# Kernel optimization log

Hardware: AMD Instinct MI355X
Metric: run time of the kernel (lower is better)

Reference implementation:

```python
import jax, jax.numpy as jnp
import numpy as np

C = 64
CQ = C // 8


def setup_inputs() -> dict:
    key = jax.random.key(0)
    ks = jax.random.split(key, 8)
    scale = 0.05
    x = jax.random.normal(ks[0], (4, C, 64, 64), dtype=jnp.float32)
    Wq = jax.random.normal(ks[1], (CQ, C), dtype=jnp.float32) * scale
    bq = jax.random.normal(ks[2], (CQ,), dtype=jnp.float32) * scale
    Wk = jax.random.normal(ks[3], (CQ, C), dtype=jnp.float32) * scale
    bk = jax.random.normal(ks[4], (CQ,), dtype=jnp.float32) * scale
    Wv = jax.random.normal(ks[5], (C, C), dtype=jnp.float32) * scale
    bv = jax.random.normal(ks[6], (C,), dtype=jnp.float32) * scale
    gamma = jnp.zeros((1,), dtype=jnp.float32) + 0.5  # nonzero so output depends on attention
    return {"x": x, "Wq": Wq, "bq": bq, "Wk": Wk, "bk": bk, "Wv": Wv, "bv": bv, "gamma": gamma}


def reference(x, Wq, bq, Wk, bk, Wv, bv, gamma):
    bs, c, h, w = x.shape
    hw = h * w
    xf = x.reshape(bs, c, hw)  # [b, c, hw]
    # 1x1 convs == per-pixel linear over channels
    Q = jnp.einsum('oc,bcn->bon', Wq, xf) + bq[None, :, None]  # [b, c/8, hw]
    K = jnp.einsum('oc,bcn->bon', Wk, xf) + bk[None, :, None]  # [b, c/8, hw]
    V = jnp.einsum('oc,bcn->bon', Wv, xf) + bv[None, :, None]  # [b, c, hw]
    # attention = softmax(Q^T K, axis=-1), NO scaling (matches source)
    scores = jnp.einsum('bqn,bqm->bnm', Q, K)  # [b, hw, hw]
    attn = jax.nn.softmax(scores, axis=-1)
    out = jnp.einsum('bcm,bmn->bcn', V, attn)  # torch.bmm(V_, attention)
    out = out.reshape(bs, c, h, w)
    return gamma[0] * out + x
```

## Files before the change

### kernel.cpp

```cpp
#include <hip/hip_runtime.h>


constexpr int Bn = 4, Cc = 64, Q8 = 8, Np = 4096;
constexpr int QK_STR = 32;
constexpr int PSTR = 40;
constexpr int NSL = 4;
constexpr int KSTR = 40;

typedef float f32x4 __attribute__((ext_vector_type(4)));
typedef short short8 __attribute__((ext_vector_type(8)));

__device__ inline unsigned int f2bf(float x) {
    unsigned int u = __float_as_uint(x);
    u += 0x7fff + ((u >> 16) & 1);
    return u >> 16;
}
__device__ inline float bf2f(unsigned int u) { return __uint_as_float(u << 16); }

__global__ __launch_bounds__(64) void qkv_v2(
    const float* __restrict__ x,
    const float* __restrict__ Wq, const float* __restrict__ bq,
    const float* __restrict__ Wk, const float* __restrict__ bk,
    const float* __restrict__ Wv, const float* __restrict__ bv,
    unsigned short* __restrict__ Qp, unsigned short* __restrict__ Kp,
    unsigned short* __restrict__ Vb)
{
    const int lane = threadIdx.x;
    const int gpos = blockIdx.x * 64;
    const int os = blockIdx.y;
    const int b = gpos >> 12, n = (gpos & (Np - 1)) + lane;

    float xv[Cc];
    const float* xp = x + (size_t)(b * Cc) * Np + n;
    #pragma unroll
    for (int c = 0; c < Cc; c++) xv[c] = xp[(size_t)c * Np];

    if (os == 0) {
        unsigned pk[4];
        float a0, a1;
        #pragma unroll
        for (int p = 0; p < 4; p++) {
            a0 = bq[2 * p]; a1 = bq[2 * p + 1];
            #pragma unroll
            for (int c = 0; c < Cc; c++) {
                a0 += Wq[(2 * p) * Cc + c] * xv[c];
                a1 += Wq[(2 * p + 1) * Cc + c] * xv[c];
            }
            pk[p] = f2bf(a0) | (f2bf(a1) << 16);
        }
        unsigned short* qrow = Qp + (size_t)(b * Np + n) * QK_STR;
        *(uint4*)qrow = make_uint4(pk[0], pk[1], pk[2], pk[3]);
        *(uint4*)(qrow + 8)  = make_uint4(0, 0, 0, 0);
        *(uint4*)(qrow + 16) = make_uint4(0, 0, 0, 0);
        *(uint4*)(qrow + 24) = make_uint4(0, 0, 0, 0);
        #pragma unroll
        for (int p = 0; p < 4; p++) {
            a0 = bk[2 * p]; a1 = bk[2 * p + 1];
            #pragma unroll
            for (int c = 0; c < Cc; c++) {
                a0 += Wk[(2 * p) * Cc + c] * xv[c];
                a1 += Wk[(2 * p + 1) * Cc + c] * xv[c];
            }
            pk[p] = f2bf(a0) | (f2bf(a1) << 16);
        }
        unsigned short* krow = Kp + (size_t)(b * Np + n) * QK_STR;
        *(uint4*)krow = make_uint4(pk[0], pk[1], pk[2], pk[3]);
        *(uint4*)(krow + 8)  = make_uint4(0, 0, 0, 0);
        *(uint4*)(krow + 16) = make_uint4(0, 0, 0, 0);
        *(uint4*)(krow + 24) = make_uint4(0, 0, 0, 0);
        #pragma unroll
        for (int o = 0; o < 4; o++) {
            float a = bv[o];
            #pragma unroll
            for (int c = 0; c < Cc; c++) a += Wv[o * Cc + c] * xv[c];
            Vb[(size_t)(b * Cc + o) * Np + n] = (unsigned short)f2bf(a);
        }
    } else {
        const int vbase = os * 20 - 16;
        #pragma unroll 4
        for (int o = 0; o < 20; o++) {
            const int vr = vbase + o;
            float a = bv[vr];
            #pragma unroll
            for (int c = 0; c < Cc; c++) a += Wv[vr * Cc + c] * xv[c];
            Vb[(size_t)(b * Cc + vr) * Np + n] = (unsigned short)f2bf(a);
        }
    }
}

__global__ __launch_bounds__(256) void zsum_v2(
    const unsigned short* __restrict__ Qp, const unsigned short* __restrict__ Kp,
    float* __restrict__ ZP)
{
    __shared__ unsigned short Klds[64 * KSTR];
    const int tid = threadIdx.x, w = tid >> 6, lane = tid & 63;
    const int quad = lane >> 4, l15 = lane & 15;
    const int bz = blockIdx.z, ns = blockIdx.y;
    const int m0 = blockIdx.x * 64 + w * 16;

    short8 qa = *(const short8*)&Qp[((size_t)(bz * Np + m0 + l15)) * QK_STR + quad * 8];

    const int rt = tid >> 2, ct = tid & 3;
    const int nbase = ns * (Np / NSL);
    const unsigned short* kbase = Kp + (size_t)bz * Np * QK_STR;

    uint4 pf = *(const uint4*)&kbase[(size_t)(nbase + rt) * QK_STR + ct * 8];
    float z0 = 0.f, z1 = 0.f, z2 = 0.f, z3 = 0.f;
    for (int nt = 0; nt < Np / NSL; nt += 64) {
        *(uint4*)&Klds[rt * KSTR + ct * 8] = pf;
        __syncthreads();
        if (nt + 64 < Np / NSL)
            pf = *(const uint4*)&kbase[(size_t)(nbase + nt + 64 + rt) * QK_STR + ct * 8];
        #pragma unroll
        for (int t16 = 0; t16 < 4; t16++) {
            short8 kb = *(const short8*)&Klds[(t16 * 16 + l15) * KSTR + quad * 8];
            f32x4 s = __builtin_amdgcn_mfma_f32_16x16x32_bf16(
                qa, kb, f32x4{0.f, 0.f, 0.f, 0.f}, 0, 0, 0);
            z0 += __expf(s[0]); z1 += __expf(s[1]);
            z2 += __expf(s[2]); z3 += __expf(s[3]);
        }
        __syncthreads();
    }
    #pragma unroll
    for (int mask = 1; mask < 16; mask <<= 1) {
        z0 += __shfl_xor(z0, mask); z1 += __shfl_xor(z1, mask);
        z2 += __shfl_xor(z2, mask); z3 += __shfl_xor(z3, mask);
    }
    if (l15 == 0) {
        float4 v = make_float4(z0, z1, z2, z3);
        *(float4*)&ZP[((size_t)(bz * NSL + ns)) * Np + m0 + quad * 4] = v;
    }
}

__global__ __launch_bounds__(256) void zred(
    const float* __restrict__ ZP, float* __restrict__ Zinv)
{
    int i = blockIdx.x * 256 + threadIdx.x;
    int b = i >> 12, m = i & (Np - 1);
    float z = 0.f;
    #pragma unroll
    for (int s = 0; s < NSL; s++) z += ZP[((size_t)(b * NSL + s)) * Np + m];
    Zinv[(size_t)b * Np + m] = 1.f / z;
}

__global__ __launch_bounds__(256) void attn_mfma(
    const unsigned short* __restrict__ Qp, const unsigned short* __restrict__ Kp,
    const unsigned short* __restrict__ Vb, const float* __restrict__ Zinv,
    unsigned short* __restrict__ PO, int Ms, int SL)
{
    __shared__ unsigned short Plds[128 * PSTR];
    const int tid = threadIdx.x, w = tid >> 6, lane = tid & 63;
    const int quad = lane >> 4, l15 = lane & 15;
    const int bz = blockIdx.z, by = blockIdx.y, nb = blockIdx.x * 128;

    short8 kf[2];
    #pragma unroll
    for (int t = 0; t < 2; t++) {
        int n = nb + (2 * w + t) * 16 + l15;
        kf[t] = *(const short8*)&Kp[((size_t)(bz * Np + n)) * QK_STR + quad * 8];
    }
    f32x4 acc[4][2];
    #pragma unroll
    for (int ct = 0; ct < 4; ct++)
        #pragma unroll
        for (int t = 0; t < 2; t++) acc[ct][t] = f32x4{0.f, 0.f, 0.f, 0.f};

    const int m_base = by * Ms;
    for (int mi = 0; mi < Ms; mi += 32) {
        const int m0 = m_base + mi;
        #pragma unroll
        for (int mt = 0; mt < 2; mt++) {
            short8 qa = *(const short8*)
                &Qp[((size_t)(bz * Np + m0 + mt * 16 + l15)) * QK_STR + quad * 8];
            float4 zi = *(const float4*)
                &Zinv[(size_t)bz * Np + m0 + mt * 16 + quad * 4];
            #pragma unroll
            for (int t = 0; t < 2; t++) {
                f32x4 s = __builtin_amdgcn_mfma_f32_16x16x32_bf16(
                    qa, kf[t], f32x4{0.f, 0.f, 0.f, 0.f}, 0, 0, 0);
                unsigned e0 = f2bf(__expf(s[0]) * zi.x), e1 = f2bf(__expf(s[1]) * zi.y);
                unsigned e2 = f2bf(__expf(s[2]) * zi.z), e3 = f2bf(__expf(s[3]) * zi.w);
                int nl = (2 * w + t) * 16 + l15;
                *(uint2*)&Plds[nl * PSTR + mt * 16 + quad * 4] =
                    make_uint2(e0 | (e1 << 16), e2 | (e3 << 16));
            }
        }
        short8 pb[2];
        #pragma unroll
        for (int t = 0; t < 2; t++)
            pb[t] = *(const short8*)&Plds[(w * 32 + t * 16 + l15) * PSTR + quad * 8];
        #pragma unroll
        for (int ct = 0; ct < 4; ct++) {
            short8 ua = *(const short8*)
                &Vb[((size_t)(bz * Cc + ct * 16 + l15)) * Np + m0 + quad * 8];
            #pragma unroll
            for (int t = 0; t < 2; t++)
                acc[ct][t] = __builtin_amdgcn_mfma_f32_16x16x32_bf16(
                    ua, pb[t], acc[ct][t], 0, 0, 0);
        }
    }
    unsigned short* po = PO + ((size_t)((bz * SL + by) * Cc)) * Np + nb;
    #pragma unroll
    for (int ct = 0; ct < 4; ct++)
        #pragma unroll
        for (int t = 0; t < 2; t++) {
            int c = ct * 16 + quad * 4, n = w * 32 + t * 16 + l15;
            #pragma unroll
            for (int r = 0; r < 4; r++)
                po[(size_t)(c + r) * Np + n] = (unsigned short)f2bf(acc[ct][t][r]);
        }
}

__global__ __launch_bounds__(256) void combine_kernel(
    const unsigned short* __restrict__ PO, const float* __restrict__ x,
    const float* __restrict__ gamma, float* __restrict__ out, int sl2)
{
    int idx8 = (blockIdx.x * 256 + threadIdx.x) * 8;
    int b = idx8 >> 18;
    int c = (idx8 >> 12) & 63;
    int n = idx8 & (Np - 1);
    float o[8];
    #pragma unroll
    for (int i = 0; i < 8; i++) o[i] = 0.f;
    for (int sl = 0; sl < sl2; ++sl) {
        uint4 u = *(const uint4*)&PO[(size_t)((b * sl2 + sl) * Cc + c) * Np + n];
        o[0] += bf2f(u.x & 0xffff); o[1] += bf2f(u.x >> 16);
        o[2] += bf2f(u.y & 0xffff); o[3] += bf2f(u.y >> 16);
        o[4] += bf2f(u.z & 0xffff); o[5] += bf2f(u.z >> 16);
        o[6] += bf2f(u.w & 0xffff); o[7] += bf2f(u.w >> 16);
    }
    float g = gamma[0];
    float4 x0 = *(const float4*)&x[idx8];
    float4 x1 = *(const float4*)&x[idx8 + 4];
    float4 r0 = make_float4(g * o[0] + x0.x, g * o[1] + x0.y,
                            g * o[2] + x0.z, g * o[3] + x0.w);
    float4 r1 = make_float4(g * o[4] + x1.x, g * o[5] + x1.y,
                            g * o[6] + x1.z, g * o[7] + x1.w);
    *(float4*)&out[idx8] = r0;
    *(float4*)&out[idx8 + 4] = r1;
}

extern "C" void kernel_launch(void* const* d_in, const int* in_sizes, int n_in,
                              void* d_out, int out_size, void* d_ws, size_t ws_size,
                              hipStream_t stream)
{
    const float* x     = (const float*)d_in[0];
    const float* Wq    = (const float*)d_in[1];
    const float* bq    = (const float*)d_in[2];
    const float* Wk    = (const float*)d_in[3];
    const float* bk    = (const float*)d_in[4];
    const float* Wv    = (const float*)d_in[5];
    const float* bv    = (const float*)d_in[6];
    const float* gamma = (const float*)d_in[7];
    float* out = (float*)d_out;

    unsigned short* Qp = (unsigned short*)d_ws;
    unsigned short* Kp = Qp + (size_t)Bn * Np * QK_STR;
    unsigned short* Vb = Kp + (size_t)Bn * Np * QK_STR;
    float* Zinv = (float*)(Vb + (size_t)Bn * Cc * Np);
    float* ZP   = Zinv + (size_t)Bn * Np;
    unsigned short* PO = (unsigned short*)(ZP + (size_t)Bn * NSL * Np);

    size_t baseB = (size_t)Bn * Np * QK_STR * 2 * 2 + (size_t)Bn * Cc * Np * 2
                 + (size_t)Bn * Np * 4 + (size_t)Bn * NSL * Np * 4;
    int SL = 4;
    while (SL > 1 && baseB + (size_t)Bn * SL * Cc * Np * 2 > ws_size) SL >>= 1;

    qkv_v2<<<dim3(Bn * Np / 64, 4), 64, 0, stream>>>(x, Wq, bq, Wk, bk, Wv, bv,
                                                     Qp, Kp, Vb);
    zsum_v2<<<dim3(Np / 64, NSL, Bn), 256, 0, stream>>>(Qp, Kp, ZP);
    zred<<<Bn * Np / 256, 256, 0, stream>>>(ZP, Zinv);
    attn_mfma<<<dim3(Np / 128, SL, Bn), 256, 0, stream>>>(Qp, Kp, Vb, Zinv,
                                                          PO, Np / SL, SL);
    combine_kernel<<<Bn * Cc * Np / (256 * 8), 256, 0, stream>>>(PO, x, gamma, out, SL);
}
```

Measured before the change: 149.4 us.

## Fold softmax normalizer into MFMA accumulator via log2 and halve attn tile

Q is prescaled by log2(e) so exponentials become native exp2, and the per-row normalizer is stored as -log2(Z) and fed as the MFMA accumulator init, which removes the separate multiply by 1/Z. Packing to bf16 now uses the hardware v_cvt_pk_bf16_f32 instruction instead of manual rounding. The attention block drops from 128 to 64 columns, so each wave handles a single 16-column tile, which doubles the block count but halves per-wave work and also doubles the reloads of Q and V across blocks.

```diff
diff --git a/kernel.cpp b/kernel.cpp
--- a/kernel.cpp
+++ b/kernel.cpp
@@ -16,6 +16,26 @@
     return u >> 16;
 }
 __device__ inline float bf2f(unsigned int u) { return __uint_as_float(u << 16); }
+
+__device__ inline unsigned cvt_pk_bf16(float a, float b) {
+    unsigned r;
+    asm("v_cvt_pk_bf16_f32 %0, %1, %2" : "=v"(r) : "v"(a), "v"(b));
+    return r;
+}
+__device__ inline float exp2g(float x) {
+#if __has_builtin(__builtin_amdgcn_exp2f)
+    return __builtin_amdgcn_exp2f(x);
+#else
+    return exp2f(x);
+#endif
+}
+__device__ inline float log2g(float x) {
+#if __has_builtin(__builtin_amdgcn_logf)
+    return __builtin_amdgcn_logf(x);
+#else
+    return log2f(x);
+#endif
+}
 
 __global__ __launch_bounds__(64) void qkv_v2(
     const float* __restrict__ x,
@@ -29,6 +49,7 @@
     const int gpos = blockIdx.x * 64;
     const int os = blockIdx.y;
     const int b = gpos >> 12, n = (gpos & (Np - 1)) + lane;
+    const float LOG2E = 1.4426950408889634f;
 
     float xv[Cc];
     const float* xp = x + (size_t)(b * Cc) * Np + n;
@@ -46,7 +67,7 @@
                 a0 += Wq[(2 * p) * Cc + c] * xv[c];
                 a1 += Wq[(2 * p + 1) * Cc + c] * xv[c];
             }
-            pk[p] = f2bf(a0) | (f2bf(a1) << 16);
+            pk[p] = f2bf(a0 * LOG2E) | (f2bf(a1 * LOG2E) << 16);
         }
         unsigned short* qrow = Qp + (size_t)(b * Np + n) * QK_STR;
         *(uint4*)qrow = make_uint4(pk[0], pk[1], pk[2], pk[3]);
@@ -116,8 +137,8 @@
             short8 kb = *(const short8*)&Klds[(t16 * 16 + l15) * KSTR + quad * 8];
             f32x4 s = __builtin_amdgcn_mfma_f32_16x16x32_bf16(
                 qa, kb, f32x4{0.f, 0.f, 0.f, 0.f}, 0, 0, 0);
-            z0 += __expf(s[0]); z1 += __expf(s[1]);
-            z2 += __expf(s[2]); z3 += __expf(s[3]);
+            z0 += exp2g(s[0]); z1 += exp2g(s[1]);
+            z2 += exp2g(s[2]); z3 += exp2g(s[3]);
         }
         __syncthreads();
     }
@@ -133,37 +154,32 @@
 }
 
 __global__ __launch_bounds__(256) void zred(
-    const float* __restrict__ ZP, float* __restrict__ Zinv)
+    const float* __restrict__ ZP, float* __restrict__ Lg)
 {
     int i = blockIdx.x * 256 + threadIdx.x;
     int b = i >> 12, m = i & (Np - 1);
     float z = 0.f;
     #pragma unroll
     for (int s = 0; s < NSL; s++) z += ZP[((size_t)(b * NSL + s)) * Np + m];
-    Zinv[(size_t)b * Np + m] = 1.f / z;
-}
-
-__global__ __launch_bounds__(256) void attn_mfma(
+    Lg[(size_t)b * Np + m] = -log2g(z);
+}
+
+__global__ __launch_bounds__(256) void attn_v2(
     const unsigned short* __restrict__ Qp, const unsigned short* __restrict__ Kp,
-    const unsigned short* __restrict__ Vb, const float* __restrict__ Zinv,
+    const unsigned short* __restrict__ Vb, const float* __restrict__ Lg,
     unsigned short* __restrict__ PO, int Ms, int SL)
 {
-    __shared__ unsigned short Plds[128 * PSTR];
+    __shared__ unsigned short Plds[64 * PSTR];
     const int tid = threadIdx.x, w = tid >> 6, lane = tid & 63;
     const int quad = lane >> 4, l15 = lane & 15;
-    const int bz = blockIdx.z, by = blockIdx.y, nb = blockIdx.x * 128;
-
-    short8 kf[2];
-    #pragma unroll
-    for (int t = 0; t < 2; t++) {
-        int n = nb + (2 * w + t) * 16 + l15;
-        kf[t] = *(const short8*)&Kp[((size_t)(bz * Np + n)) * QK_STR + quad * 8];
-    }
-    f32x4 acc[4][2];
-    #pragma unroll
-    for (int ct = 0; ct < 4; ct++)
-        #pragma unroll
-        for (int t = 0; t < 2; t++) acc[ct][t] = f32x4{0.f, 0.f, 0.f, 0.f};
+    const int bz = blockIdx.z, by = blockIdx.y, nb = blockIdx.x * 64;
+    const int nl = w * 16 + l15;
+
+    short8 kf = *(const short8*)&Kp[((size_t)(bz * Np + nb + nl)) * QK_STR + quad * 8];
+
+    f32x4 acc[4];
+    #pragma unroll
+    for (int ct = 0; ct < 4; ct++) acc[ct] = f32x4{0.f, 0.f, 0.f, 0.f};
 
     const int m_base = by * Ms;
     for (int mi = 0; mi < Ms; mi += 32) {
@@ -172,43 +188,29 @@
         for (int mt = 0; mt < 2; mt++) {
             short8 qa = *(const short8*)
                 &Qp[((size_t)(bz * Np + m0 + mt * 16 + l15)) * QK_STR + quad * 8];
-            float4 zi = *(const float4*)
-                &Zinv[(size_t)bz * Np + m0 + mt * 16 + quad * 4];
-            #pragma unroll
-            for (int t = 0; t < 2; t++) {
-                f32x4 s = __builtin_amdgcn_mfma_f32_16x16x32_bf16(
-                    qa, kf[t], f32x4{0.f, 0.f, 0.f, 0.f}, 0, 0, 0);
-                unsigned e0 = f2bf(__expf(s[0]) * zi.x), e1 = f2bf(__expf(s[1]) * zi.y);
-                unsigned e2 = f2bf(__expf(s[2]) * zi.z), e3 = f2bf(__expf(s[3]) * zi.w);
-                int nl = (2 * w + t) * 16 + l15;
-                *(uint2*)&Plds[nl * PSTR + mt * 16 + quad * 4] =
-                    make_uint2(e0 | (e1 << 16), e2 | (e3 << 16));
-            }
-        }
-        short8 pb[2];
-        #pragma unroll
-        for (int t = 0; t < 2; t++)
-            pb[t] = *(const short8*)&Plds[(w * 32 + t * 16 + l15) * PSTR + quad * 8];
+            f32x4 Lc = *(const f32x4*)
+                &Lg[(size_t)bz * Np + m0 + mt * 16 + quad * 4];
+            f32x4 s = __builtin_amdgcn_mfma_f32_16x16x32_bf16(qa, kf, Lc, 0, 0, 0);
+            unsigned p01 = cvt_pk_bf16(exp2g(s[0]), exp2g(s[1]));
+            unsigned p23 = cvt_pk_bf16(exp2g(s[2]), exp2g(s[3]));
+            *(uint2*)&Plds[nl * PSTR + mt * 16 + quad * 4] = make_uint2(p01, p23);
+        }
+        short8 pb = *(const short8*)&Plds[nl * PSTR + quad * 8];
         #pragma unroll
         for (int ct = 0; ct < 4; ct++) {
             short8 ua = *(const short8*)
                 &Vb[((size_t)(bz * Cc + ct * 16 + l15)) * Np + m0 + quad * 8];
-            #pragma unroll
-            for (int t = 0; t < 2; t++)
-                acc[ct][t] = __builtin_amdgcn_mfma_f32_16x16x32_bf16(
-                    ua, pb[t], acc[ct][t], 0, 0, 0);
+            acc[ct] = __builtin_amdgcn_mfma_f32_16x16x32_bf16(ua, pb, acc[ct], 0, 0, 0);
         }
     }
     unsigned short* po = PO + ((size_t)((bz * SL + by) * Cc)) * Np + nb;
     #pragma unroll
-    for (int ct = 0; ct < 4; ct++)
-        #pragma unroll
-        for (int t = 0; t < 2; t++) {
-            int c = ct * 16 + quad * 4, n = w * 32 + t * 16 + l15;
-            #pragma unroll
-            for (int r = 0; r < 4; r++)
-                po[(size_t)(c + r) * Np + n] = (unsigned short)f2bf(acc[ct][t][r]);
-        }
+    for (int ct = 0; ct < 4; ct++) {
+        int c = ct * 16 + quad * 4;
+        #pragma unroll
+        for (int r = 0; r < 4; r++)
+            po[(size_t)(c + r) * Np + nl] = (unsigned short)f2bf(acc[ct][r]);
+    }
 }
 
 __global__ __launch_bounds__(256) void combine_kernel(
@@ -257,8 +259,8 @@
     unsigned short* Qp = (unsigned short*)d_ws;
     unsigned short* Kp = Qp + (size_t)Bn * Np * QK_STR;
     unsigned short* Vb = Kp + (size_t)Bn * Np * QK_STR;
-    float* Zinv = (float*)(Vb + (size_t)Bn * Cc * Np);
-    float* ZP   = Zinv + (size_t)Bn * Np;
+    float* Lg   = (float*)(Vb + (size_t)Bn * Cc * Np);
+    float* ZP   = Lg + (size_t)Bn * Np;
     unsigned short* PO = (unsigned short*)(ZP + (size_t)Bn * NSL * Np);
 
     size_t baseB = (size_t)Bn * Np * QK_STR * 2 * 2 + (size_t)Bn * Cc * Np * 2
@@ -269,8 +271,8 @@
     qkv_v2<<<dim3(Bn * Np / 64, 4), 64, 0, stream>>>(x, Wq, bq, Wk, bk, Wv, bv,
                                                      Qp, Kp, Vb);
     zsum_v2<<<dim3(Np / 64, NSL, Bn), 256, 0, stream>>>(Qp, Kp, ZP);
-    zred<<<Bn * Np / 256, 256, 0, stream>>>(ZP, Zinv);
-    attn_mfma<<<dim3(Np / 128, SL, Bn), 256, 0, stream>>>(Qp, Kp, Vb, Zinv,
-                                                          PO, Np / SL, SL);
+    zred<<<Bn * Np / 256, 256, 0, stream>>>(ZP, Lg);
+    attn_v2<<<dim3(Np / 64, SL, Bn), 256, 0, stream>>>(Qp, Kp, Vb, Lg,
+                                                       PO, Np / SL, SL);
     combine_kernel<<<Bn * Cc * Np / (256 * 8), 256, 0, stream>>>(PO, x, gamma, out, SL);
 }
```

Result: slower. 185.0 us (+23.8%).
